# Kernel tuning notes

Hardware: AMD Instinct MI355X
Metric: run time of the kernel (lower is better)

The kernel has to match this reference:

```python
import jax, jax.numpy as jnp
import numpy as np

B, NT, DIM, HEADS = 8, 16, 768, 8
RES_H = RES_W = 32
PIX = RES_H * RES_W              # 1024
CHAN_NH = 16
NH = NW = 4                      # sqrt(chan_nheads)
WH, WW = RES_H // NH, RES_W // NW  # 8, 8
HEAD_DIM = DIM // HEADS          # 96
CHAN_HEAD_DIM = PIX // CHAN_NH   # 64


def _linear(x, w, b=None):
    y = x @ w.T
    return y if b is None else y + b


def _quat_kernel(r, i, j, k):
    # Hamilton-product block kernel: (4*out_c, 4*in_c, K)
    row_r = jnp.concatenate([r, -i, -j, -k], axis=1)
    row_i = jnp.concatenate([i, r, -k, j], axis=1)
    row_j = jnp.concatenate([j, k, r, -i], axis=1)
    row_k = jnp.concatenate([k, -j, i, r], axis=1)
    return jnp.concatenate([row_r, row_i, row_j, row_k], axis=0)


def _conv1d(x, w, b=None, pad=1):
    y = jax.lax.conv_general_dilated(x, w, (1,), [(pad, pad)],
                                     dimension_numbers=('NCH', 'OIH', 'NCH'))
    return y if b is None else y + b[None, :, None]


def _win(z, t):
    # 'b t (nh h nw w) -> b (nh nw) t (h w)'
    b = z.shape[0]
    z = z.reshape(b, t, NH, WH, NW, WW).transpose(0, 2, 4, 1, 3, 5)
    return z.reshape(b, NH * NW, t, WH * WW)


def setup_inputs():
    key = jax.random.key(0)
    ks = jax.random.split(key, 24)
    s = lambda i, shape: jax.random.normal(ks[i], shape, dtype=jnp.float32) * 0.02
    return dict(
        x=jax.random.normal(ks[0], (B, PIX, DIM), jnp.float32),
        task_prompts=jax.random.normal(ks[1], (B, NT, DIM), jnp.float32),
        qkv_w=s(2, (3 * DIM, DIM)),
        proj_w=s(3, (DIM, DIM)), proj_b=s(4, (DIM,)),
        tt_w=s(5, (PIX, DIM)), tt_b=s(6, (PIX,)),
        tt1_w=s(7, (DIM, PIX)), tt1_b=s(8, (DIM,)),
        qf_r=s(9, (2, 1, 3)), qf_i=s(10, (2, 1, 3)), qf_j=s(11, (2, 1, 3)),
        qf_k=s(12, (2, 1, 3)), qf_b=s(13, (8,)),
        dqf_r=s(14, (2, 1, 3)), dqf_i=s(15, (2, 1, 3)), dqf_j=s(16, (2, 1, 3)),
        dqf_k=s(17, (2, 1, 3)), dqf_b=s(18, (4,)),
        bn_g=jnp.ones((4,), jnp.float32), bn_b=jnp.zeros((4,), jnp.float32),
        qfto_w=s(19, (1, 4, 1)),
    )


def reference(x, task_prompts, qkv_w, proj_w, proj_b, tt_w, tt_b, tt1_w, tt1_b,
              qf_r, qf_i, qf_j, qf_k, qf_b, dqf_r, dqf_i, dqf_j, dqf_k, dqf_b,
              bn_g, bn_b, qfto_w):
    # ---- spatial attention over [prompts ; pixels] ----
    xc = jnp.concatenate([task_prompts, x], axis=1)           # (B, N, C), N = NT + PIX
    b, n, c = xc.shape
    qkv = _linear(xc, qkv_w).reshape(b, n, 3, HEADS, HEAD_DIM).transpose(2, 0, 3, 1, 4)
    q, k, v = qkv[0], qkv[1], qkv[2]
    raw_spa = jnp.einsum('bhqd,bhkd->bhqk', q, k)             # pre-scale logits (returned)
    spa_attn = jax.nn.softmax(raw_spa * HEAD_DIM ** -0.5, axis=-1)
    out = jnp.einsum('bhqk,bhkd->bhqd', spa_attn, v).transpose(0, 2, 1, 3).reshape(b, n, c)
    out = _linear(out, proj_w, proj_b)
    tp_out, x_out = out[:, :-PIX, :], out[:, -PIX:, :]        # sep_prompt(x, -pixel_no)

    # ---- windowed channel attention ----
    chan_x = x[:, -PIX:, :]                                   # (B, PIX, C)
    chan_prompts = _linear(task_prompts, tt_w, tt_b)          # (B, NT, PIX)
    qw = _win(chan_prompts, NT)                               # (B, 16, NT, 64)
    kw = _win(chan_x.transpose(0, 2, 1), DIM)                 # (B, 16, C, 64)
    raw_chan = jnp.einsum('bwtd,bwcd->bwtc', qw, kw)          # (B, 16, NT, C)
    chan_attn = jax.nn.softmax(raw_chan * CHAN_HEAD_DIM ** -0.5, axis=-1)
    # chan_x output of attn@v is computed in torch but unused downstream; XLA DCEs it.
    raw_chan_r = raw_chan.reshape(b, NH, NW, NT, DIM).transpose(0, 3, 4, 1, 2)   # b t c nh nw
    chan_attn_r = chan_attn.reshape(b, NH, NW, NT, DIM).transpose(0, 3, 4, 1, 2)

    # ---- quaternion fusion of prompt streams (vectorized over the torch per-sample loop) ----
    ch_prompts = _linear(chan_prompts, tt1_w, tt1_b)          # (B, NT, C)
    zero = jnp.zeros_like(tp_out)
    quater = jnp.stack([zero, task_prompts, tp_out, ch_prompts], axis=2)  # (B, NT, 4, C)
    w1 = _quat_kernel(qf_r, qf_i, qf_j, qf_k)                 # (8, 4, 3), OIH
    fe = _conv1d(quater.reshape(b * NT, 4, DIM), w1, qf_b)    # (B*NT, 8, C)
    w2 = _quat_kernel(dqf_r, dqf_i, dqf_j, dqf_k)             # (8, 4, 3) as (in, out, K)
    w2c = jnp.flip(w2, -1).transpose(1, 0, 2)                 # conv_transpose1d(s=1,p=1) == conv1d(flip, p=K-1-1)
    fe = _conv1d(fe, w2c, dqf_b).reshape(b, NT, 4, DIM)       # (B, NT, 4, C)
    # BatchNorm1d(4) in training mode, stats per loop iteration => per-sample over (NT, C)
    mean = fe.mean(axis=(1, 3), keepdims=True)
    var = fe.var(axis=(1, 3), keepdims=True)
    fe = (fe - mean) / jnp.sqrt(var + 1e-5) * bn_g[None, None, :, None] + bn_b[None, None, :, None]
    fe = jax.nn.gelu(fe, approximate=False)
    quater_out = jnp.einsum('bnkc,k->bnc', fe, qfto_w[0, :, 0])  # Conv1d(4,1,k=1,no bias)
    return (x_out, raw_spa, spa_attn, raw_chan_r, chan_attn_r, quater_out)
```

## Files before the change

### kernel.cpp

```cpp
#include <hip/hip_runtime.h>
#include <hip/hip_bf16.h>
#include <math.h>

typedef unsigned short u16;
typedef __attribute__((ext_vector_type(8))) short  bf16x8;
typedef __attribute__((ext_vector_type(4))) float  f32x4;
typedef __attribute__((ext_vector_type(8))) u16    u16x8;
typedef __attribute__((ext_vector_type(4))) u16    u16x4;

#define B_      8
#define NT_     16
#define DIM_    768
#define HEADS_  8
#define HD_     96
#define PIX_    1024
#define NTOK_   1040
#define NPAD_   1152

#define WSO_XCB     0ull
#define WSO_WQKV    12779520ull
#define WSO_WPROJ   16318464ull
#define WSO_QB      17498112ull
#define WSO_KB      31653888ull
#define WSO_VB      45809664ull
#define WSO_VTB     59965440ull
#define WSO_ACATB   74121216ull
#define WSO_TPB     86900736ull
#define WSO_TTWB    87097344ull
#define WSO_TT1WB   88670208ull
#define WSO_CHANPB  90243072ull
#define WSO_PART    90505216ull
#define WSO_F32     95813632ull
#define FO_TPOUT    0ull
#define FO_RAWCHAN  98304ull
#define FO_CHP      1671168ull
#define FO_FE2      1769472ull
#define FO_STATS    2162688ull

#define OUT_XOUT   0ull
#define OUT_RAW    6291456ull
#define OUT_ATTN   75513856ull
#define OUT_RAWCH  144736256ull
#define OUT_ATTNCH 146309120ull
#define OUT_QOUT   147881984ull

#define SCALE_SPA 0.1020620726159658f

__device__ __forceinline__ u16 f2b(float f) {
    union { float f; unsigned u; } x; x.f = f;
    unsigned r = x.u + 0x7FFFu + ((x.u >> 16) & 1u);
    return (u16)(r >> 16);
}
__device__ __forceinline__ u16 f2b_fast(float f) {
    __hip_bfloat16 h = __float2bfloat16(f);
    return __builtin_bit_cast(u16, h);
}
__device__ __forceinline__ float b2f(u16 h) {
    union { unsigned u; float f; } x; x.u = ((unsigned)h) << 16;
    return x.f;
}

__global__ __launch_bounds__(256) void cast_concat(const float* __restrict__ tp,
                                                   const float* __restrict__ x,
                                                   u16* __restrict__ xcb) {
    size_t idx8 = ((size_t)blockIdx.x * 256 + threadIdx.x) * 8;
    int c = idx8 % DIM_;
    int n = (idx8 / DIM_) % NTOK_;
    int b = idx8 / ((size_t)DIM_ * NTOK_);
    const float* s = (n < NT_) ? tp + ((size_t)b * NT_ + n) * DIM_ + c
                               : x + ((size_t)b * PIX_ + (n - NT_)) * DIM_ + c;
    float4 a = *(const float4*)s;
    float4 d = *(const float4*)(s + 4);
    u16x8 r;
    r[0] = f2b(a.x); r[1] = f2b(a.y); r[2] = f2b(a.z); r[3] = f2b(a.w);
    r[4] = f2b(d.x); r[5] = f2b(d.y); r[6] = f2b(d.z); r[7] = f2b(d.w);
    *(u16x8*)(xcb + idx8) = r;
}

__global__ __launch_bounds__(256) void cast_all(const float* __restrict__ qkv_w,
                                                const float* __restrict__ proj_w,
                                                const float* __restrict__ tp,
                                                const float* __restrict__ tt_w,
                                                const float* __restrict__ tt1_w,
                                                u16* __restrict__ wqkvb,
                                                u16* __restrict__ wprojb,
                                                u16* __restrict__ tpb,
                                                u16* __restrict__ ttwb,
                                                u16* __restrict__ tt1wb) {
    int i = blockIdx.x * 256 + threadIdx.x;
    const float* src;
    u16* dst;
    int li;
    if (i < 221184)      { src = qkv_w;  dst = wqkvb;  li = i; }
    else if (i < 294912) { src = proj_w; dst = wprojb; li = i - 221184; }
    else if (i < 307200) { src = tp;     dst = tpb;    li = i - 294912; }
    else if (i < 405504) { src = tt_w;   dst = ttwb;   li = i - 307200; }
    else if (i < 503808) { src = tt1_w;  dst = tt1wb;  li = i - 405504; }
    else return;
    const float* s = src + (size_t)li * 8;
    float4 a = *(const float4*)s;
    float4 d = *(const float4*)(s + 4);
    u16x8 r;
    r[0] = f2b(a.x); r[1] = f2b(a.y); r[2] = f2b(a.z); r[3] = f2b(a.w);
    r[4] = f2b(d.x); r[5] = f2b(d.y); r[6] = f2b(d.z); r[7] = f2b(d.w);
    *(u16x8*)(dst + (size_t)li * 8) = r;
}

template <int MODE>
__global__ __launch_bounds__(256) void gemm_bf16(
    const u16* __restrict__ A, const u16* __restrict__ Bw,
    int lda, int ldb, int K, size_t strA, size_t strB,
    const float* __restrict__ bias,
    float* __restrict__ o0, float* __restrict__ o1,
    u16* __restrict__ oq, u16* __restrict__ ok, u16* __restrict__ ov,
    int ldo) {
    __shared__ u16 As[128][40];
    __shared__ u16 Bs[128][40];
    __shared__ float redm[128][2];
    __shared__ float reds[128][2];
    const int tid = threadIdx.x;
    const int bm = blockIdx.x, bn = blockIdx.y, z = blockIdx.z;
    const u16* Ab = A + strA * z;
    const u16* Bb = Bw + strB * z;
    const int lane = tid & 63, wid = tid >> 6;
    const int ln = lane & 15, hi = lane >> 4;
    const int wr = wid >> 1, wc = wid & 1;
    const int srow = tid >> 1, scol = (tid & 1) * 16;
    f32x4 acc[4][4] = {};
    for (int kt = 0; kt < K; kt += 32) {
        __syncthreads();
        const u16* ga = Ab + (size_t)(bm * 128 + srow) * lda + kt + scol;
        const u16* gb = Bb + (size_t)(bn * 128 + srow) * ldb + kt + scol;
        u16x8 a0 = *(const u16x8*)ga, a1 = *(const u16x8*)(ga + 8);
        u16x8 b0 = *(const u16x8*)gb, b1 = *(const u16x8*)(gb + 8);
        *(u16x8*)&As[srow][scol] = a0;
        *(u16x8*)&As[srow][scol + 8] = a1;
        *(u16x8*)&Bs[srow][scol] = b0;
        *(u16x8*)&Bs[srow][scol + 8] = b1;
        __syncthreads();
        bf16x8 af[4], bfr[4];
#pragma unroll
        for (int m = 0; m < 4; ++m) af[m] = *(const bf16x8*)&As[wr * 64 + m * 16 + ln][hi * 8];
#pragma unroll
        for (int n = 0; n < 4; ++n) bfr[n] = *(const bf16x8*)&Bs[wc * 64 + n * 16 + ln][hi * 8];
#pragma unroll
        for (int m = 0; m < 4; ++m)
#pragma unroll
            for (int n = 0; n < 4; ++n)
                acc[m][n] = __builtin_amdgcn_mfma_f32_16x16x32_bf16(af[m], bfr[n], acc[m][n], 0, 0, 0);
    }
#pragma unroll
    for (int m = 0; m < 4; ++m) {
#pragma unroll
        for (int n = 0; n < 4; ++n) {
#pragma unroll
            for (int j = 0; j < 4; ++j) {
                int gm = bm * 128 + wr * 64 + m * 16 + hi * 4 + j;
                int gn = bn * 128 + wc * 64 + n * 16 + ln;
                float v = acc[m][n][j];
                if (MODE == 0) {
                    int b = gm / NTOK_, nn = gm - b * NTOK_;
                    int s = gn / DIM_, rem = gn - s * DIM_;
                    int h = rem / HD_, d = rem - h * HD_;
                    u16 hv = f2b(v);
                    u16* dst = (s == 0) ? oq : (s == 1) ? ok : ov;
                    dst[(((size_t)b * HEADS_ + h) * NPAD_ + nn) * HD_ + d] = hv;
                } else if (MODE == 1) {
                    if (gm < NTOK_ && gn < NTOK_)
                        __builtin_nontemporal_store(v, &o0[((size_t)z * NTOK_ + gm) * NTOK_ + gn]);
                } else if (MODE == 2) {
                    v += bias[gn];
                    int b = gm / NTOK_, nn = gm - b * NTOK_;
                    if (nn < NT_) o1[((size_t)b * NT_ + nn) * DIM_ + gn] = v;
                    else          __builtin_nontemporal_store(v, &o0[((size_t)b * PIX_ + (nn - NT_)) * DIM_ + gn]);
                } else if (MODE == 3) {
                    oq[(size_t)gm * ldo + gn] = f2b(v + bias[gn]);
                } else {
                    o0[(size_t)gm * ldo + gn] = v + bias[gn];
                }
            }
        }
    }
    if (MODE == 1) {
#pragma unroll
        for (int m = 0; m < 4; ++m) {
#pragma unroll
            for (int j = 0; j < 4; ++j) {
                float v[4];
                float mx = -INFINITY;
#pragma unroll
                for (int n = 0; n < 4; ++n) {
                    int gn = bn * 128 + wc * 64 + n * 16 + ln;
                    v[n] = (gn < NTOK_) ? acc[m][n][j] * SCALE_SPA : -INFINITY;
                    mx = fmaxf(mx, v[n]);
                }
#pragma unroll
                for (int off = 1; off < 16; off <<= 1) mx = fmaxf(mx, __shfl_xor(mx, off));
                float s = 0.f;
                if (mx > -INFINITY) {
#pragma unroll
                    for (int n = 0; n < 4; ++n)
                        if (v[n] > -INFINITY) s += __expf(v[n] - mx);
                }
#pragma unroll
                for (int off = 1; off < 16; off <<= 1) s += __shfl_xor(s, off);
                if (ln == 0) {
                    int row = wr * 64 + m * 16 + hi * 4 + j;
                    redm[row][wc] = mx;
                    reds[row][wc] = s;
                }
            }
        }
        __syncthreads();
        if (tid < 128) {
            float m0 = redm[tid][0], m1 = redm[tid][1];
            float s0 = reds[tid][0], s1 = reds[tid][1];
            float M = fmaxf(m0, m1);
            float S = 0.f;
            if (m0 > -INFINITY) S += s0 * __expf(m0 - M);
            if (m1 > -INFINITY) S += s1 * __expf(m1 - M);
            float2* pp = (float2*)o1;
            pp[((size_t)z * 9 + bn) * NPAD_ + bm * 128 + tid] = make_float2(M, S);
        }
    }
}

__global__ __launch_bounds__(256) void transpose_v(const u16* __restrict__ vb,
                                                   u16* __restrict__ vtb) {
    __shared__ u16 t[32][34];
    int bi = blockIdx.x, bj = blockIdx.y, z = blockIdx.z;
    const u16* ib = vb + (size_t)z * NPAD_ * HD_;
    u16* ob = vtb + (size_t)z * HD_ * NPAD_;
    int tid = threadIdx.x;
    int r = tid >> 3, c = (tid & 7) * 4;
    *(u16x4*)&t[r][c] = *(const u16x4*)(ib + (size_t)(bi * 32 + r) * HD_ + bj * 32 + c);
    __syncthreads();
    u16x4 o;
    o[0] = t[c + 0][r]; o[1] = t[c + 1][r]; o[2] = t[c + 2][r]; o[3] = t[c + 3][r];
    *(u16x4*)(ob + (size_t)(bj * 32 + r) * NPAD_ + bi * 32 + c) = o;
}

__global__ __launch_bounds__(256) void attn_pv3(const float* __restrict__ raw,
                                                const float2* __restrict__ part,
                                                const u16* __restrict__ vtb,
                                                float* __restrict__ attn,
                                                u16* __restrict__ acat) {
    __shared__ u16 Ps[32][136];
    __shared__ float sm[32], si[32];
    const int tid = threadIdx.x;
    const int bi = blockIdx.x, z = blockIdx.y;
    if (tid < 32) {
        int grow = bi * 32 + tid;
        float M = -INFINITY;
        float mj[9], sj[9];
#pragma unroll
        for (int jt = 0; jt < 9; ++jt) {
            float2 p = part[((size_t)z * 9 + jt) * NPAD_ + grow];
            mj[jt] = p.x; sj[jt] = p.y;
            M = fmaxf(M, p.x);
        }
        float S = 0.f;
#pragma unroll
        for (int jt = 0; jt < 9; ++jt)
            if (mj[jt] > -INFINITY) S += sj[jt] * __expf(mj[jt] - M);
        sm[tid] = M;
        si[tid] = 1.f / S;
    }
    __syncthreads();
    const int lane = tid & 63, wid = tid >> 6;
    const int ln = lane & 15, hi = lane >> 4;
    const int wr = wid >> 1, wc = wid & 1;
    const int r = tid >> 3, c8 = tid & 7;
    const int grow = bi * 32 + r;
    const bool vrow = grow < NTOK_;
    const float* rp = raw + (size_t)z * NTOK_ * NTOK_ + (size_t)(vrow ? grow : 0) * NTOK_;
    float* aw = attn + (size_t)z * NTOK_ * NTOK_ + (size_t)(vrow ? grow : 0) * NTOK_;
    const u16* vbz = vtb + (size_t)z * HD_ * NPAD_;
    const float m_r = sm[r], inv_r = si[r];
    f32x4 oacc[3] = {};
    for (int c0 = 0; c0 < 1056; c0 += 128) {
        const int nsub = (c0 == 1024) ? 1 : 4;
#pragma unroll 4
        for (int s = 0; s < nsub; ++s) {
            int cl = s * 32 + c8 * 4;
            int col = c0 + cl;
            bool okc = vrow && (col < NTOK_);
            u16x4 pb = {0, 0, 0, 0};
            if (okc) {
                f32x4 v = __builtin_nontemporal_load((const f32x4*)(rp + col));
                f32x4 p;
                p[0] = __expf(v[0] * SCALE_SPA - m_r) * inv_r;
                p[1] = __expf(v[1] * SCALE_SPA - m_r) * inv_r;
                p[2] = __expf(v[2] * SCALE_SPA - m_r) * inv_r;
                p[3] = __expf(v[3] * SCALE_SPA - m_r) * inv_r;
                __builtin_nontemporal_store(p, (f32x4*)(aw + col));
                pb[0] = f2b_fast(p[0]); pb[1] = f2b_fast(p[1]);
                pb[2] = f2b_fast(p[2]); pb[3] = f2b_fast(p[3]);
            }
            *(u16x4*)&Ps[r][cl] = pb;
        }
        __syncthreads();
#pragma unroll 4
        for (int ktl = 0; ktl < nsub; ++ktl) {
            bf16x8 af = *(const bf16x8*)&Ps[wr * 16 + ln][ktl * 32 + hi * 8];
#pragma unroll
            for (int n = 0; n < 3; ++n) {
                bf16x8 bv = *(const bf16x8*)(vbz + (size_t)(wc * 48 + n * 16 + ln) * NPAD_
                                             + c0 + ktl * 32 + hi * 8);
                oacc[n] = __builtin_amdgcn_mfma_f32_16x16x32_bf16(af, bv, oacc[n], 0, 0, 0);
            }
        }
        __syncthreads();
    }
    const int b = z >> 3, h = z & 7;
#pragma unroll
    for (int n = 0; n < 3; ++n)
#pragma unroll
        for (int j = 0; j < 4; ++j) {
            int gi = bi * 32 + wr * 16 + hi * 4 + j;
            if (gi < NTOK_) {
                int gd = wc * 48 + n * 16 + ln;
                acat[((size_t)b * NTOK_ + gi) * DIM_ + h * HD_ + gd] = f2b(oacc[n][j]);
            }
        }
}

__global__ __launch_bounds__(256) void chan_scores(const u16* __restrict__ chanpb,
                                                   const float* __restrict__ x,
                                                   float* __restrict__ rawchan_ws,
                                                   float* __restrict__ out_raw) {
    int blk = blockIdx.x;
    int b = blk / 16, w = blk % 16;
    int cy = blockIdx.y;
    int nh = w / 4, nw = w % 4;
    __shared__ float qp[16][65];
    __shared__ float xs[64][17];
    int tid = threadIdx.x;
    for (int l = tid; l < 16 * 64; l += 256) {
        int t = l / 64, d = l % 64;
        int wh = d / 8, ww = d % 8;
        int pix = (nh * 8 + wh) * 32 + nw * 8 + ww;
        qp[t][d] = b2f(chanpb[((size_t)b * NT_ + t) * PIX_ + pix]);
    }
    __syncthreads();
    int t = tid % 16, cl = tid / 16;
    for (int cc = cy * 8; cc < cy * 8 + 8; ++cc) {
        for (int l = tid; l < 64 * 16; l += 256) {
            int d = l / 16, c2 = l % 16;
            int wh = d / 8, ww = d % 8;
            int pix = (nh * 8 + wh) * 32 + nw * 8 + ww;
            xs[d][c2] = x[((size_t)b * PIX_ + pix) * DIM_ + cc * 16 + c2];
        }
        __syncthreads();
        float acc = 0.f;
#pragma unroll
        for (int d = 0; d < 64; ++d) acc += qp[t][d] * xs[d][cl];
        int c = cc * 16 + cl;
        rawchan_ws[(((size_t)b * 16 + w) * NT_ + t) * DIM_ + c] = acc;
        out_raw[(((size_t)b * NT_ + t) * DIM_ + c) * 16 + w] = acc;
        __syncthreads();
    }
}

__global__ __launch_bounds__(256) void chan_softmax(const float* __restrict__ rawchan_ws,
                                                    float* __restrict__ out_attn) {
    int row = blockIdx.x;
    int b = row / 256;
    int w = (row / 16) % 16;
    int t = row % 16;
    const float* rp = rawchan_ws + (size_t)row * DIM_;
    int tid = threadIdx.x;
    float vals[3];
    float m = -INFINITY;
#pragma unroll
    for (int i = 0; i < 3; ++i) {
        vals[i] = rp[tid + i * 256] * 0.125f;
        m = fmaxf(m, vals[i]);
    }
    __shared__ float redm[4], reds[4];
    for (int off = 32; off; off >>= 1) m = fmaxf(m, __shfl_xor(m, off));
    if ((tid & 63) == 0) redm[tid >> 6] = m;
    __syncthreads();
    m = fmaxf(fmaxf(redm[0], redm[1]), fmaxf(redm[2], redm[3]));
    float s = 0.f;
#pragma unroll
    for (int i = 0; i < 3; ++i) { vals[i] = __expf(vals[i] - m); s += vals[i]; }
    for (int off = 32; off; off >>= 1) s += __shfl_xor(s, off);
    if ((tid & 63) == 0) reds[tid >> 6] = s;
    __syncthreads();
    s = reds[0] + reds[1] + reds[2] + reds[3];
    float inv = 1.f / s;
#pragma unroll
    for (int i = 0; i < 3; ++i) {
        int c = tid + i * 256;
        out_attn[(((size_t)b * NT_ + t) * DIM_ + c) * 16 + w] = vals[i] * inv;
    }
}

__global__ __launch_bounds__(256) void quat_conv(const float* __restrict__ tp,
                                                 const float* __restrict__ tpo,
                                                 const float* __restrict__ chp,
                                                 const float* __restrict__ qf_r, const float* __restrict__ qf_i,
                                                 const float* __restrict__ qf_j, const float* __restrict__ qf_k,
                                                 const float* __restrict__ qf_b,
                                                 const float* __restrict__ dqf_r, const float* __restrict__ dqf_i,
                                                 const float* __restrict__ dqf_j, const float* __restrict__ dqf_k,
                                                 const float* __restrict__ dqf_b,
                                                 float* __restrict__ fe2_out,
                                                 float* __restrict__ partials) {
    int blk = blockIdx.x;
    int b = blk / NT_, t = blk % NT_;
    __shared__ float w1[8][4][3];
    __shared__ float w2[8][4][3];
    __shared__ float w2c[4][8][3];
    __shared__ float qs[4][770];
    __shared__ float fs[8][770];
    __shared__ float wsum[4][4], wsq[4][4];
    int tid = threadIdx.x;
    if (tid < 96) {
        int o = tid / 12, rest = tid % 12, ic = rest / 3, tap = rest % 3;
        int g = o / 2, oo = o % 2;
        const int   cidx[4][4] = {{0, 1, 2, 3}, {1, 0, 3, 2}, {2, 3, 0, 1}, {3, 2, 1, 0}};
        const float csgn[4][4] = {{1, -1, -1, -1}, {1, 1, -1, 1}, {1, 1, 1, -1}, {1, -1, 1, 1}};
        const float* s1[4] = {qf_r, qf_i, qf_j, qf_k};
        const float* s2[4] = {dqf_r, dqf_i, dqf_j, dqf_k};
        w1[o][ic][tap] = csgn[g][ic] * s1[cidx[g][ic]][oo * 3 + tap];
        w2[o][ic][tap] = csgn[g][ic] * s2[cidx[g][ic]][oo * 3 + tap];
    }
    for (int l = tid; l < DIM_; l += 256) {
        size_t base = ((size_t)b * NT_ + t) * DIM_ + l;
        qs[0][1 + l] = 0.f;
        qs[1][1 + l] = tp[base];
        qs[2][1 + l] = tpo[base];
        qs[3][1 + l] = chp[base];
    }
    if (tid < 4) { qs[tid][0] = 0.f; qs[tid][769] = 0.f; }
    if (tid < 8) { fs[tid][0] = 0.f; fs[tid][769] = 0.f; }
    __syncthreads();
    if (tid < 96) {
        int o2 = tid / 24, rest = tid % 24, i2 = rest / 3, tap = rest % 3;
        w2c[o2][i2][tap] = w2[i2][o2][2 - tap];
    }
    for (int l = tid; l < DIM_; l += 256) {
#pragma unroll
        for (int o = 0; o < 8; ++o) {
            float a = qf_b[o];
#pragma unroll
            for (int ic = 0; ic < 4; ++ic)
#pragma unroll
                for (int tap = 0; tap < 3; ++tap) a += w1[o][ic][tap] * qs[ic][l + tap];
            fs[o][1 + l] = a;
        }
    }
    __syncthreads();
    float lsum[4] = {}, lsq[4] = {};
    for (int l = tid; l < DIM_; l += 256) {
#pragma unroll
        for (int o2 = 0; o2 < 4; ++o2) {
            float a = dqf_b[o2];
#pragma unroll
            for (int i2 = 0; i2 < 8; ++i2)
#pragma unroll
                for (int tap = 0; tap < 3; ++tap) a += w2c[o2][i2][tap] * fs[i2][l + tap];
            fe2_out[((size_t)blk * 4 + o2) * DIM_ + l] = a;
            lsum[o2] += a;
            lsq[o2] += a * a;
        }
    }
    int wid = tid >> 6;
#pragma unroll
    for (int o2 = 0; o2 < 4; ++o2) {
        float s = lsum[o2], q = lsq[o2];
        for (int off = 32; off; off >>= 1) { s += __shfl_xor(s, off); q += __shfl_xor(q, off); }
        if ((tid & 63) == 0) { wsum[wid][o2] = s; wsq[wid][o2] = q; }
    }
    __syncthreads();
    if (tid < 4) {
        float s = wsum[0][tid] + wsum[1][tid] + wsum[2][tid] + wsum[3][tid];
        float q = wsq[0][tid] + wsq[1][tid] + wsq[2][tid] + wsq[3][tid];
        partials[(size_t)blk * 8 + tid * 2 + 0] = s;
        partials[(size_t)blk * 8 + tid * 2 + 1] = q;
    }
}

__global__ __launch_bounds__(256) void bn_gelu_out(const float* __restrict__ fe2,
                                                   const float* __restrict__ partials,
                                                   const float* __restrict__ bn_g,
                                                   const float* __restrict__ bn_b,
                                                   const float* __restrict__ qfto,
                                                   float* __restrict__ out5) {
    int blk = blockIdx.x;
    int b = blk / NT_;
    int tid = threadIdx.x;
    float mean[4], rstd[4], gam[4], bet[4], qw[4];
#pragma unroll
    for (int kk = 0; kk < 4; ++kk) {
        float s = 0.f, q = 0.f;
        for (int t2 = 0; t2 < 16; ++t2) {
            const float* p = partials + ((size_t)(b * NT_ + t2) * 8 + kk * 2);
            s += p[0];
            q += p[1];
        }
        float mu = s * (1.f / 12288.f);
        float var = q * (1.f / 12288.f) - mu * mu;
        mean[kk] = mu;
        rstd[kk] = rsqrtf(var + 1e-5f);
        gam[kk] = bn_g[kk];
        bet[kk] = bn_b[kk];
        qw[kk] = qfto[kk];
    }
    for (int l = tid; l < DIM_; l += 256) {
        float acc = 0.f;
#pragma unroll
        for (int kk = 0; kk < 4; ++kk) {
            float v = fe2[((size_t)blk * 4 + kk) * DIM_ + l];
            float nrm = (v - mean[kk]) * rstd[kk] * gam[kk] + bet[kk];
            float ge = 0.5f * nrm * (1.f + erff(nrm * 0.7071067811865475f));
            acc += ge * qw[kk];
        }
        out5[(size_t)blk * DIM_ + l] = acc;
    }
}

extern "C" void kernel_launch(void* const* d_in, const int* in_sizes, int n_in,
                              void* d_out, int out_size, void* d_ws, size_t ws_size,
                              hipStream_t stream) {
    const float* x      = (const float*)d_in[0];
    const float* tp     = (const float*)d_in[1];
    const float* qkv_w  = (const float*)d_in[2];
    const float* proj_w = (const float*)d_in[3];
    const float* proj_b = (const float*)d_in[4];
    const float* tt_w   = (const float*)d_in[5];
    const float* tt_b   = (const float*)d_in[6];
    const float* tt1_w  = (const float*)d_in[7];
    const float* tt1_b  = (const float*)d_in[8];
    const float* qf_r   = (const float*)d_in[9];
    const float* qf_i   = (const float*)d_in[10];
    const float* qf_j   = (const float*)d_in[11];
    const float* qf_k   = (const float*)d_in[12];
    const float* qf_b   = (const float*)d_in[13];
    const float* dqf_r  = (const float*)d_in[14];
    const float* dqf_i  = (const float*)d_in[15];
    const float* dqf_j  = (const float*)d_in[16];
    const float* dqf_k  = (const float*)d_in[17];
    const float* dqf_b  = (const float*)d_in[18];
    const float* bn_g   = (const float*)d_in[19];
    const float* bn_b   = (const float*)d_in[20];
    const float* qfto   = (const float*)d_in[21];
    float* out = (float*)d_out;
    char* wsb = (char*)d_ws;

    u16* xcb    = (u16*)(wsb + WSO_XCB);
    u16* wqkvb  = (u16*)(wsb + WSO_WQKV);
    u16* wprojb = (u16*)(wsb + WSO_WPROJ);
    u16* qb     = (u16*)(wsb + WSO_QB);
    u16* kb     = (u16*)(wsb + WSO_KB);
    u16* vb     = (u16*)(wsb + WSO_VB);
    u16* vtb    = (u16*)(wsb + WSO_VTB);
    u16* acatb  = (u16*)(wsb + WSO_ACATB);
    u16* tpb    = (u16*)(wsb + WSO_TPB);
    u16* ttwb   = (u16*)(wsb + WSO_TTWB);
    u16* tt1wb  = (u16*)(wsb + WSO_TT1WB);
    u16* chanpb = (u16*)(wsb + WSO_CHANPB);
    float* partb = (float*)(wsb + WSO_PART);
    float* f32r = (float*)(wsb + WSO_F32);
    float* tpout   = f32r + FO_TPOUT;
    float* rawchan = f32r + FO_RAWCHAN;
    float* chpf    = f32r + FO_CHP;
    float* fe2     = f32r + FO_FE2;
    float* stats   = f32r + FO_STATS;

    cast_concat<<<3120, 256, 0, stream>>>(tp, x, xcb);
    cast_all<<<1968, 256, 0, stream>>>(qkv_w, proj_w, tp, tt_w, tt1_w,
                                       wqkvb, wprojb, tpb, ttwb, tt1wb);

    gemm_bf16<0><<<dim3(65, 18, 1), 256, 0, stream>>>(xcb, wqkvb, 768, 768, 768, 0, 0,
                                                      nullptr, nullptr, nullptr, qb, kb, vb, 0);
    transpose_v<<<dim3(36, 3, 64), 256, 0, stream>>>(vb, vtb);
    gemm_bf16<1><<<dim3(9, 9, 64), 256, 0, stream>>>(qb, kb, 96, 96, 96,
                                                     (size_t)NPAD_ * HD_, (size_t)NPAD_ * HD_,
                                                     nullptr, out + OUT_RAW, partb,
                                                     nullptr, nullptr, nullptr, 0);
    attn_pv3<<<dim3(33, 64), 256, 0, stream>>>(out + OUT_RAW, (const float2*)partb,
                                               vtb, out + OUT_ATTN, acatb);
    gemm_bf16<2><<<dim3(65, 6, 1), 256, 0, stream>>>(acatb, wprojb, 768, 768, 768, 0, 0,
                                                     proj_b, out + OUT_XOUT, tpout,
                                                     nullptr, nullptr, nullptr, 0);
    gemm_bf16<3><<<dim3(1, 8, 1), 256, 0, stream>>>(tpb, ttwb, 768, 768, 768, 0, 0,
                                                    tt_b, nullptr, nullptr, chanpb, nullptr, nullptr, 1024);
    chan_scores<<<dim3(128, 6), 256, 0, stream>>>(chanpb, x, rawchan, out + OUT_RAWCH);
    chan_softmax<<<2048, 256, 0, stream>>>(rawchan, out + OUT_ATTNCH);
    gemm_bf16<4><<<dim3(1, 6, 1), 256, 0, stream>>>(chanpb, tt1wb, 1024, 1024, 1024, 0, 0,
                                                    tt1_b, chpf, nullptr, nullptr, nullptr, nullptr, 768);
    quat_conv<<<128, 256, 0, stream>>>(tp, tpout, chpf,
                                       qf_r, qf_i, qf_j, qf_k, qf_b,
                                       dqf_r, dqf_i, dqf_j, dqf_k, dqf_b,
                                       fe2, stats);
    bn_gelu_out<<<128, 256, 0, stream>>>(fe2, stats, bn_g, bn_b, qfto, out + OUT_QOUT);
}
```

Baseline: 540.8 us.

## Merge independent kernels into combined launches to cut launch count

Independent stages are grouped into shared launches that branch on block index: the two cast kernels, the QKV GEMM with the channel-prompt GEMM, the V transpose with the channel scores, and the spatial score GEMM with the channel softmax and the tt1 GEMM. This drops about six kernel launches and the serialization between them, and lets small GEMMs run alongside large ones. Channel-attention outputs now use nontemporal stores. The merged kernels carry the larger shared-memory footprint and register pressure of the GEMM path into blocks that would not otherwise need it, which can lower occupancy for the lighter work.

After: 640.7 us. 1.18x slower.

```diff
diff --git a/kernel.cpp b/kernel.cpp
--- a/kernel.cpp
+++ b/kernel.cpp
@@ -60,66 +60,21 @@
     return x.f;
 }
 
-__global__ __launch_bounds__(256) void cast_concat(const float* __restrict__ tp,
-                                                   const float* __restrict__ x,
-                                                   u16* __restrict__ xcb) {
-    size_t idx8 = ((size_t)blockIdx.x * 256 + threadIdx.x) * 8;
-    int c = idx8 % DIM_;
-    int n = (idx8 / DIM_) % NTOK_;
-    int b = idx8 / ((size_t)DIM_ * NTOK_);
-    const float* s = (n < NT_) ? tp + ((size_t)b * NT_ + n) * DIM_ + c
-                               : x + ((size_t)b * PIX_ + (n - NT_)) * DIM_ + c;
-    float4 a = *(const float4*)s;
-    float4 d = *(const float4*)(s + 4);
-    u16x8 r;
-    r[0] = f2b(a.x); r[1] = f2b(a.y); r[2] = f2b(a.z); r[3] = f2b(a.w);
-    r[4] = f2b(d.x); r[5] = f2b(d.y); r[6] = f2b(d.z); r[7] = f2b(d.w);
-    *(u16x8*)(xcb + idx8) = r;
-}
-
-__global__ __launch_bounds__(256) void cast_all(const float* __restrict__ qkv_w,
-                                                const float* __restrict__ proj_w,
-                                                const float* __restrict__ tp,
-                                                const float* __restrict__ tt_w,
-                                                const float* __restrict__ tt1_w,
-                                                u16* __restrict__ wqkvb,
-                                                u16* __restrict__ wprojb,
-                                                u16* __restrict__ tpb,
-                                                u16* __restrict__ ttwb,
-                                                u16* __restrict__ tt1wb) {
-    int i = blockIdx.x * 256 + threadIdx.x;
-    const float* src;
-    u16* dst;
-    int li;
-    if (i < 221184)      { src = qkv_w;  dst = wqkvb;  li = i; }
-    else if (i < 294912) { src = proj_w; dst = wprojb; li = i - 221184; }
-    else if (i < 307200) { src = tp;     dst = tpb;    li = i - 294912; }
-    else if (i < 405504) { src = tt_w;   dst = ttwb;   li = i - 307200; }
-    else if (i < 503808) { src = tt1_w;  dst = tt1wb;  li = i - 405504; }
-    else return;
-    const float* s = src + (size_t)li * 8;
-    float4 a = *(const float4*)s;
-    float4 d = *(const float4*)(s + 4);
-    u16x8 r;
-    r[0] = f2b(a.x); r[1] = f2b(a.y); r[2] = f2b(a.z); r[3] = f2b(a.w);
-    r[4] = f2b(d.x); r[5] = f2b(d.y); r[6] = f2b(d.z); r[7] = f2b(d.w);
-    *(u16x8*)(dst + (size_t)li * 8) = r;
-}
+struct GemmSmem {
+    u16 As[128][40];
+    u16 Bs[128][40];
+    float redm[128][2];
+    float reds[128][2];
+};
 
 template <int MODE>
-__global__ __launch_bounds__(256) void gemm_bf16(
+__device__ __forceinline__ void gemm_core(GemmSmem& sm, int tid, int bm, int bn, int z,
     const u16* __restrict__ A, const u16* __restrict__ Bw,
     int lda, int ldb, int K, size_t strA, size_t strB,
     const float* __restrict__ bias,
     float* __restrict__ o0, float* __restrict__ o1,
     u16* __restrict__ oq, u16* __restrict__ ok, u16* __restrict__ ov,
     int ldo) {
-    __shared__ u16 As[128][40];
-    __shared__ u16 Bs[128][40];
-    __shared__ float redm[128][2];
-    __shared__ float reds[128][2];
-    const int tid = threadIdx.x;
-    const int bm = blockIdx.x, bn = blockIdx.y, z = blockIdx.z;
     const u16* Ab = A + strA * z;
     const u16* Bb = Bw + strB * z;
     const int lane = tid & 63, wid = tid >> 6;
@@ -133,16 +88,16 @@
         const u16* gb = Bb + (size_t)(bn * 128 + srow) * ldb + kt + scol;
         u16x8 a0 = *(const u16x8*)ga, a1 = *(const u16x8*)(ga + 8);
         u16x8 b0 = *(const u16x8*)gb, b1 = *(const u16x8*)(gb + 8);
-        *(u16x8*)&As[srow][scol] = a0;
-        *(u16x8*)&As[srow][scol + 8] = a1;
-        *(u16x8*)&Bs[srow][scol] = b0;
-        *(u16x8*)&Bs[srow][scol + 8] = b1;
+        *(u16x8*)&sm.As[srow][scol] = a0;
+        *(u16x8*)&sm.As[srow][scol + 8] = a1;
+        *(u16x8*)&sm.Bs[srow][scol] = b0;
+        *(u16x8*)&sm.Bs[srow][scol + 8] = b1;
         __syncthreads();
         bf16x8 af[4], bfr[4];
 #pragma unroll
-        for (int m = 0; m < 4; ++m) af[m] = *(const bf16x8*)&As[wr * 64 + m * 16 + ln][hi * 8];
-#pragma unroll
-        for (int n = 0; n < 4; ++n) bfr[n] = *(const bf16x8*)&Bs[wc * 64 + n * 16 + ln][hi * 8];
+        for (int m = 0; m < 4; ++m) af[m] = *(const bf16x8*)&sm.As[wr * 64 + m * 16 + ln][hi * 8];
+#pragma unroll
+        for (int n = 0; n < 4; ++n) bfr[n] = *(const bf16x8*)&sm.Bs[wc * 64 + n * 16 + ln][hi * 8];
 #pragma unroll
         for (int m = 0; m < 4; ++m)
 #pragma unroll
@@ -206,15 +161,15 @@
                 for (int off = 1; off < 16; off <<= 1) s += __shfl_xor(s, off);
                 if (ln == 0) {
                     int row = wr * 64 + m * 16 + hi * 4 + j;
-                    redm[row][wc] = mx;
-                    reds[row][wc] = s;
+                    sm.redm[row][wc] = mx;
+                    sm.reds[row][wc] = s;
                 }
             }
         }
         __syncthreads();
         if (tid < 128) {
-            float m0 = redm[tid][0], m1 = redm[tid][1];
-            float s0 = reds[tid][0], s1 = reds[tid][1];
+            float m0 = sm.redm[tid][0], m1 = sm.redm[tid][1];
+            float s0 = sm.reds[tid][0], s1 = sm.reds[tid][1];
             float M = fmaxf(m0, m1);
             float S = 0.f;
             if (m0 > -INFINITY) S += s0 * __expf(m0 - M);
@@ -225,19 +180,187 @@
     }
 }
 
-__global__ __launch_bounds__(256) void transpose_v(const u16* __restrict__ vb,
-                                                   u16* __restrict__ vtb) {
+__global__ __launch_bounds__(256) void k_casts(const float* __restrict__ tp,
+                                               const float* __restrict__ x,
+                                               const float* __restrict__ qkv_w,
+                                               const float* __restrict__ proj_w,
+                                               const float* __restrict__ tt_w,
+                                               const float* __restrict__ tt1_w,
+                                               u16* __restrict__ xcb,
+                                               u16* __restrict__ wqkvb,
+                                               u16* __restrict__ wprojb,
+                                               u16* __restrict__ tpb,
+                                               u16* __restrict__ ttwb,
+                                               u16* __restrict__ tt1wb) {
+    int bx = blockIdx.x, tid = threadIdx.x;
+    if (bx < 3120) {
+        size_t idx8 = ((size_t)bx * 256 + tid) * 8;
+        int c = idx8 % DIM_;
+        int n = (idx8 / DIM_) % NTOK_;
+        int b = idx8 / ((size_t)DIM_ * NTOK_);
+        const float* s = (n < NT_) ? tp + ((size_t)b * NT_ + n) * DIM_ + c
+                                   : x + ((size_t)b * PIX_ + (n - NT_)) * DIM_ + c;
+        float4 a = *(const float4*)s;
+        float4 d = *(const float4*)(s + 4);
+        u16x8 r;
+        r[0] = f2b(a.x); r[1] = f2b(a.y); r[2] = f2b(a.z); r[3] = f2b(a.w);
+        r[4] = f2b(d.x); r[5] = f2b(d.y); r[6] = f2b(d.z); r[7] = f2b(d.w);
+        *(u16x8*)(xcb + idx8) = r;
+    } else {
+        int i = (bx - 3120) * 256 + tid;
+        const float* src;
+        u16* dst;
+        int li;
+        if (i < 221184)      { src = qkv_w;  dst = wqkvb;  li = i; }
+        else if (i < 294912) { src = proj_w; dst = wprojb; li = i - 221184; }
+        else if (i < 307200) { src = tp;     dst = tpb;    li = i - 294912; }
+        else if (i < 405504) { src = tt_w;   dst = ttwb;   li = i - 307200; }
+        else if (i < 503808) { src = tt1_w;  dst = tt1wb;  li = i - 405504; }
+        else return;
+        const float* s = src + (size_t)li * 8;
+        float4 a = *(const float4*)s;
+        float4 d = *(const float4*)(s + 4);
+        u16x8 r;
+        r[0] = f2b(a.x); r[1] = f2b(a.y); r[2] = f2b(a.z); r[3] = f2b(a.w);
+        r[4] = f2b(d.x); r[5] = f2b(d.y); r[6] = f2b(d.z); r[7] = f2b(d.w);
+        *(u16x8*)(dst + (size_t)li * 8) = r;
+    }
+}
+
+__global__ __launch_bounds__(256) void k_qkv_chanp(const u16* __restrict__ xcb,
+                                                   const u16* __restrict__ wqkvb,
+                                                   const u16* __restrict__ tpb,
+                                                   const u16* __restrict__ ttwb,
+                                                   const float* __restrict__ tt_b,
+                                                   u16* __restrict__ qb,
+                                                   u16* __restrict__ kb,
+                                                   u16* __restrict__ vb,
+                                                   u16* __restrict__ chanpb) {
+    __shared__ GemmSmem sm;
+    int bx = blockIdx.x, tid = threadIdx.x;
+    if (bx < 1170) {
+        gemm_core<0>(sm, tid, bx % 65, bx / 65, 0, xcb, wqkvb, 768, 768, 768, 0, 0,
+                     nullptr, nullptr, nullptr, qb, kb, vb, 0);
+    } else {
+        gemm_core<3>(sm, tid, 0, bx - 1170, 0, tpb, ttwb, 768, 768, 768, 0, 0,
+                     tt_b, nullptr, nullptr, chanpb, nullptr, nullptr, 1024);
+    }
+}
+
+__global__ __launch_bounds__(256) void k_vt_chansc(const u16* __restrict__ vb,
+                                                   u16* __restrict__ vtb,
+                                                   const u16* __restrict__ chanpb,
+                                                   const float* __restrict__ x,
+                                                   float* __restrict__ rawchan_ws,
+                                                   float* __restrict__ out_raw) {
     __shared__ u16 t[32][34];
-    int bi = blockIdx.x, bj = blockIdx.y, z = blockIdx.z;
-    const u16* ib = vb + (size_t)z * NPAD_ * HD_;
-    u16* ob = vtb + (size_t)z * HD_ * NPAD_;
-    int tid = threadIdx.x;
-    int r = tid >> 3, c = (tid & 7) * 4;
-    *(u16x4*)&t[r][c] = *(const u16x4*)(ib + (size_t)(bi * 32 + r) * HD_ + bj * 32 + c);
-    __syncthreads();
-    u16x4 o;
-    o[0] = t[c + 0][r]; o[1] = t[c + 1][r]; o[2] = t[c + 2][r]; o[3] = t[c + 3][r];
-    *(u16x4*)(ob + (size_t)(bj * 32 + r) * NPAD_ + bi * 32 + c) = o;
+    __shared__ float qp[16][65];
+    __shared__ float xs[64][17];
+    int bx = blockIdx.x, tid = threadIdx.x;
+    if (bx < 6912) {
+        int bi = bx % 36, bj = (bx / 36) % 3, z = bx / 108;
+        const u16* ib = vb + (size_t)z * NPAD_ * HD_;
+        u16* ob = vtb + (size_t)z * HD_ * NPAD_;
+        int r = tid >> 3, c = (tid & 7) * 4;
+        *(u16x4*)&t[r][c] = *(const u16x4*)(ib + (size_t)(bi * 32 + r) * HD_ + bj * 32 + c);
+        __syncthreads();
+        u16x4 o;
+        o[0] = t[c + 0][r]; o[1] = t[c + 1][r]; o[2] = t[c + 2][r]; o[3] = t[c + 3][r];
+        *(u16x4*)(ob + (size_t)(bj * 32 + r) * NPAD_ + bi * 32 + c) = o;
+    } else {
+        int idx2 = bx - 6912;
+        int blk = idx2 & 127, cy = idx2 >> 7;
+        int b = blk / 16, w = blk % 16;
+        int nh = w / 4, nw = w % 4;
+        for (int l = tid; l < 16 * 64; l += 256) {
+            int tt = l / 64, d = l % 64;
+            int wh = d / 8, ww = d % 8;
+            int pix = (nh * 8 + wh) * 32 + nw * 8 + ww;
+            qp[tt][d] = b2f(chanpb[((size_t)b * NT_ + tt) * PIX_ + pix]);
+        }
+        __syncthreads();
+        int tt = tid % 16, cl = tid / 16;
+        for (int cc = cy * 8; cc < cy * 8 + 8; ++cc) {
+            for (int l = tid; l < 64 * 16; l += 256) {
+                int d = l / 16, c2 = l % 16;
+                int wh = d / 8, ww = d % 8;
+                int pix = (nh * 8 + wh) * 32 + nw * 8 + ww;
+                xs[d][c2] = x[((size_t)b * PIX_ + pix) * DIM_ + cc * 16 + c2];
+            }
+            __syncthreads();
+            float acc = 0.f;
+#pragma unroll
+            for (int d = 0; d < 64; ++d) acc += qp[tt][d] * xs[d][cl];
+            int c = cc * 16 + cl;
+            rawchan_ws[(((size_t)b * 16 + w) * NT_ + tt) * DIM_ + c] = acc;
+            __builtin_nontemporal_store(acc, &out_raw[(((size_t)b * NT_ + tt) * DIM_ + c) * 16 + w]);
+            __syncthreads();
+        }
+    }
+}
+
+__global__ __launch_bounds__(256) void k_scores_chansm_tt1(const u16* __restrict__ qb,
+                                                           const u16* __restrict__ kb,
+                                                           float* __restrict__ raw,
+                                                           float* __restrict__ partb,
+                                                           const float* __restrict__ rawchan_ws,
+                                                           float* __restrict__ out_attn,
+                                                           const u16* __restrict__ chanpb,
+                                                           const u16* __restrict__ tt1wb,
+                                                           const float* __restrict__ tt1_b,
+                                                           float* __restrict__ chpf) {
+    __shared__ GemmSmem sm;
+    __shared__ float csm[8];
+    int bx = blockIdx.x, tid = threadIdx.x;
+    if (bx < 5184) {
+        gemm_core<1>(sm, tid, bx % 9, (bx / 9) % 9, bx / 81, qb, kb, 96, 96, 96,
+                     (size_t)NPAD_ * HD_, (size_t)NPAD_ * HD_,
+                     nullptr, raw, partb, nullptr, nullptr, nullptr, 0);
+    } else if (bx < 7232) {
+        int row = bx - 5184;
+        int b = row / 256;
+        int w = (row / 16) % 16;
+        int t = row % 16;
+        const float* rp = rawchan_ws + (size_t)row * DIM_;
+        float vals[3];
+        float m = -INFINITY;
+#pragma unroll
+        for (int i = 0; i < 3; ++i) {
+            vals[i] = rp[tid + i * 256] * 0.125f;
+            m = fmaxf(m, vals[i]);
+        }
+        for (int off = 32; off; off >>= 1) m = fmaxf(m, __shfl_xor(m, off));
+        if ((tid & 63) == 0) csm[tid >> 6] = m;
+        __syncthreads();
+        m = fmaxf(fmaxf(csm[0], csm[1]), fmaxf(csm[2], csm[3]));
+        float s = 0.f;
+#pragma unroll
+        for (int i = 0; i < 3; ++i) { vals[i] = __expf(vals[i] - m); s += vals[i]; }
+        for (int off = 32; off; off >>= 1) s += __shfl_xor(s, off);
+        if ((tid & 63) == 0) csm[4 + (tid >> 6)] = s;
+        __syncthreads();
+        s = csm[4] + csm[5] + csm[6] + csm[7];
+        float inv = 1.f / s;
+#pragma unroll
+        for (int i = 0; i < 3; ++i) {
+            int c = tid + i * 256;
+            __builtin_nontemporal_store(vals[i] * inv,
+                &out_attn[(((size_t)b * NT_ + t) * DIM_ + c) * 16 + w]);
+        }
+    } else {
+        gemm_core<4>(sm, tid, 0, bx - 7232, 0, chanpb, tt1wb, 1024, 1024, 1024, 0, 0,
+                     tt1_b, chpf, nullptr, nullptr, nullptr, nullptr, 768);
+    }
+}
+
+__global__ __launch_bounds__(256) void k_proj(const u16* __restrict__ acatb,
+                                              const u16* __restrict__ wprojb,
+                                              const float* __restrict__ proj_b,
+                                              float* __restrict__ xout,
+                                              float* __restrict__ tpout) {
+    __shared__ GemmSmem sm;
+    gemm_core<2>(sm, threadIdx.x, blockIdx.x, blockIdx.y, 0, acatb, wprojb,
+                 768, 768, 768, 0, 0, proj_b, xout, tpout, nullptr, nullptr, nullptr, 0);
 }
 
 __global__ __launch_bounds__(256) void attn_pv3(const float* __restrict__ raw,
@@ -325,78 +448,6 @@
         }
 }
 
-__global__ __launch_bounds__(256) void chan_scores(const u16* __restrict__ chanpb,
-                                                   const float* __restrict__ x,
-                                                   float* __restrict__ rawchan_ws,
-                                                   float* __restrict__ out_raw) {
-    int blk = blockIdx.x;
-    int b = blk / 16, w = blk % 16;
-    int cy = blockIdx.y;
-    int nh = w / 4, nw = w % 4;
-    __shared__ float qp[16][65];
-    __shared__ float xs[64][17];
-    int tid = threadIdx.x;
-    for (int l = tid; l < 16 * 64; l += 256) {
-        int t = l / 64, d = l % 64;
-        int wh = d / 8, ww = d % 8;
-        int pix = (nh * 8 + wh) * 32 + nw * 8 + ww;
-        qp[t][d] = b2f(chanpb[((size_t)b * NT_ + t) * PIX_ + pix]);
-    }
-    __syncthreads();
-    int t = tid % 16, cl = tid / 16;
-    for (int cc = cy * 8; cc < cy * 8 + 8; ++cc) {
-        for (int l = tid; l < 64 * 16; l += 256) {
-            int d = l / 16, c2 = l % 16;
-            int wh = d / 8, ww = d % 8;
-            int pix = (nh * 8 + wh) * 32 + nw * 8 + ww;
-            xs[d][c2] = x[((size_t)b * PIX_ + pix) * DIM_ + cc * 16 + c2];
-        }
-        __syncthreads();
-        float acc = 0.f;
-#pragma unroll
-        for (int d = 0; d < 64; ++d) acc += qp[t][d] * xs[d][cl];
-        int c = cc * 16 + cl;
-        rawchan_ws[(((size_t)b * 16 + w) * NT_ + t) * DIM_ + c] = acc;
-        out_raw[(((size_t)b * NT_ + t) * DIM_ + c) * 16 + w] = acc;
-        __syncthreads();
-    }
-}
-
-__global__ __launch_bounds__(256) void chan_softmax(const float* __restrict__ rawchan_ws,
-                                                    float* __restrict__ out_attn) {
-    int row = blockIdx.x;
-    int b = row / 256;
-    int w = (row / 16) % 16;
-    int t = row % 16;
-    const float* rp = rawchan_ws + (size_t)row * DIM_;
-    int tid = threadIdx.x;
-    float vals[3];
-    float m = -INFINITY;
-#pragma unroll
-    for (int i = 0; i < 3; ++i) {
-        vals[i] = rp[tid + i * 256] * 0.125f;
-        m = fmaxf(m, vals[i]);
-    }
-    __shared__ float redm[4], reds[4];
-    for (int off = 32; off; off >>= 1) m = fmaxf(m, __shfl_xor(m, off));
-    if ((tid & 63) == 0) redm[tid >> 6] = m;
-    __syncthreads();
-    m = fmaxf(fmaxf(redm[0], redm[1]), fmaxf(redm[2], redm[3]));
-    float s = 0.f;
-#pragma unroll
-    for (int i = 0; i < 3; ++i) { vals[i] = __expf(vals[i] - m); s += vals[i]; }
-    for (int off = 32; off; off >>= 1) s += __shfl_xor(s, off);
-    if ((tid & 63) == 0) reds[tid >> 6] = s;
-    __syncthreads();
-    s = reds[0] + reds[1] + reds[2] + reds[3];
-    float inv = 1.f / s;
-#pragma unroll
-    for (int i = 0; i < 3; ++i) {
-        int c = tid + i * 256;
-        out_attn[(((size_t)b * NT_ + t) * DIM_ + c) * 16 + w] = vals[i] * inv;
-    }
-}
-
 __global__ __launch_bounds__(256) void quat_conv(const float* __restrict__ tp,
                                                  const float* __restrict__ tpo,
                                                  const float* __restrict__ chp,
@@ -570,28 +621,16 @@
     float* fe2     = f32r + FO_FE2;
     float* stats   = f32r + FO_STATS;
 
-    cast_concat<<<3120, 256, 0, stream>>>(tp, x, xcb);
-    cast_all<<<1968, 256, 0, stream>>>(qkv_w, proj_w, tp, tt_w, tt1_w,
-                                       wqkvb, wprojb, tpb, ttwb, tt1wb);
-
-    gemm_bf16<0><<<dim3(65, 18, 1), 256, 0, stream>>>(xcb, wqkvb, 768, 768, 768, 0, 0,
-                                                      nullptr, nullptr, nullptr, qb, kb, vb, 0);
-    transpose_v<<<dim3(36, 3, 64), 256, 0, stream>>>(vb, vtb);
-    gemm_bf16<1><<<dim3(9, 9, 64), 256, 0, stream>>>(qb, kb, 96, 96, 96,
-                                                     (size_t)NPAD_ * HD_, (size_t)NPAD_ * HD_,
-                                                     nullptr, out + OUT_RAW, partb,
-                                                     nullptr, nullptr, nullptr, 0);
+    k_casts<<<5088, 256, 0, stream>>>(tp, x, qkv_w, proj_w, tt_w, tt1_w,
+                                      xcb, wqkvb, wprojb, tpb, ttwb, tt1wb);
+    k_qkv_chanp<<<1178, 256, 0, stream>>>(xcb, wqkvb, tpb, ttwb, tt_b, qb, kb, vb, chanpb);
+    k_vt_chansc<<<7680, 256, 0, stream>>>(vb, vtb, chanpb, x, rawchan, out + OUT_RAWCH);
+    k_scores_chansm_tt1<<<7238, 256, 0, stream>>>(qb, kb, out + OUT_RAW, partb,
+                                                  rawchan, out + OUT_ATTNCH,
+                                                  chanpb, tt1wb, tt1_b, chpf);
     attn_pv3<<<dim3(33, 64), 256, 0, stream>>>(out + OUT_RAW, (const float2*)partb,
                                                vtb, out + OUT_ATTN, acatb);
-    gemm_bf16<2><<<dim3(65, 6, 1), 256, 0, stream>>>(acatb, wprojb, 768, 768, 768, 0, 0,
-                                                     proj_b, out + OUT_XOUT, tpout,
-                                                     nullptr, nullptr, nullptr, 0);
-    gemm_bf16<3><<<dim3(1, 8, 1), 256, 0, stream>>>(tpb, ttwb, 768, 768, 768, 0, 0,
-                                                    tt_b, nullptr, nullptr, chanpb, nullptr, nullptr, 1024);
-    chan_scores<<<dim3(128, 6), 256, 0, stream>>>(chanpb, x, rawchan, out + OUT_RAWCH);
-    chan_softmax<<<2048, 256, 0, stream>>>(rawchan, out + OUT_ATTNCH);
-    gemm_bf16<4><<<dim3(1, 6, 1), 256, 0, stream>>>(chanpb, tt1wb, 1024, 1024, 1024, 0, 0,
-                                                    tt1_b, chpf, nullptr, nullptr, nullptr, nullptr, 768);
+    k_proj<<<dim3(65, 6), 256, 0, stream>>>(acatb, wprojb, proj_b, out + OUT_XOUT, tpout);
     quat_conv<<<128, 256, 0, stream>>>(tp, tpout, chpf,
                                        qf_r, qf_i, qf_j, qf_k, qf_b,
                                        dqf_r, dqf_i, dqf_j, dqf_k, dqf_b,
```
